# Kernel tuning notes

Hardware: AMD Instinct MI355X
Metric: run time of the kernel (lower is better)

## Reference

```python
import jax, jax.numpy as jnp
import numpy as np

HID = 128      # hidden_dim
HEADS = 8      # num_heads
PHD = 16       # per_head_dim
NTYPES = 3     # num_edge_types
N = 50000      # num nodes
E = 250000     # edges per edge type


def setup_inputs() -> dict:
    key = jax.random.key(0)
    ks = jax.random.split(key, 8)
    x = jax.random.normal(ks[0], (N, HID), dtype=jnp.float32)
    adj0 = jax.random.randint(ks[1], (E, 2), 0, N)
    adj1 = jax.random.randint(ks[2], (E, 2), 0, N)
    adj2 = jax.random.randint(ks[3], (E, 2), 0, N)
    # weights stored [in, out] so application is x @ W (same math as torch Linear)
    Wq = jax.random.normal(ks[4], (NTYPES, HID, HEADS * PHD), dtype=jnp.float32) * 0.05
    Wk = jax.random.normal(ks[5], (NTYPES, HID, HEADS * PHD), dtype=jnp.float32) * 0.05
    Wm = jax.random.normal(ks[6], (NTYPES, 2 * HID, HEADS * PHD), dtype=jnp.float32) * 0.05
    bm = jax.random.normal(ks[7], (NTYPES, HEADS * PHD), dtype=jnp.float32) * 0.01
    return {"x": x, "adj0": adj0, "adj1": adj1, "adj2": adj2,
            "Wq": Wq, "Wk": Wk, "Wm": Wm, "bm": bm}


def reference(x, adj0, adj1, adj2, Wq, Wk, Wm, bm):
    scale = PHD ** (-0.5)
    n = x.shape[0]
    msgs, scores, tgts = [], [], []
    for t, adj in enumerate((adj0, adj1, adj2)):
        src_r = x[adj[:, 0]]                       # [E, HID]
        tgt_r = x[adj[:, 1]]                       # [E, HID]
        pair = jnp.concatenate([src_r, tgt_r], axis=1)      # [E, 2*HID]
        m = jax.nn.relu(pair @ Wm[t] + bm[t]).reshape(-1, HEADS, PHD)
        q = (tgt_r @ Wq[t]).reshape(-1, HEADS, PHD) * scale
        k = (src_r @ Wk[t]).reshape(-1, HEADS, PHD)
        s = jnp.einsum('ehd,ehd->eh', q, k)        # [E, HEADS]
        msgs.append(m); scores.append(s); tgts.append(adj[:, 1])
    all_m = jnp.concatenate(msgs, axis=0)          # [TE, HEADS, PHD]
    all_s = jnp.concatenate(scores, axis=0)        # [TE, HEADS]
    all_t = jnp.concatenate(tgts, axis=0)          # [TE]
    # segment log-softmax over edges grouped by target node
    smax = jax.ops.segment_max(all_s, all_t, num_segments=n)        # [N, HEADS]
    shifted = all_s - smax[all_t]
    sumexp = jax.ops.segment_sum(jnp.exp(shifted), all_t, num_segments=n)
    logZ = jnp.log(jnp.where(sumexp > 0, sumexp, 1.0))
    probs = jnp.exp(shifted - logZ[all_t])                          # [TE, HEADS]
    agg = jax.ops.segment_sum(probs[..., None] * all_m, all_t, num_segments=n)
    return agg.reshape(n, HEADS * PHD)
```

## Files before the change

### kernel.cpp

```cpp
#include <hip/hip_runtime.h>

#define HID 128
#define NE 250000
#define NT 3
#define NN 50000
#define CAP 48
#define BPAD 136
#define PLANE (NN * 256)
#define GEMM_BLOCKS 391
#define EDGE_BLOCKS ((NT * NE + 511) / 512)

typedef unsigned int u32;
typedef unsigned short u16;
typedef __attribute__((ext_vector_type(8))) short short8;
typedef __attribute__((ext_vector_type(4))) float f32x4;

__device__ __forceinline__ u16 f2bf(float f) {
    u32 u = __float_as_uint(f);
    u += 0x7fffu + ((u >> 16) & 1u);
    return (u16)(u >> 16);
}
__device__ __forceinline__ float bflo(u32 u) { return __uint_as_float(u << 16); }
__device__ __forceinline__ float bfhi(u32 u) { return __uint_as_float(u & 0xffff0000u); }

__device__ __forceinline__ short8 pack8(const float4 a, const float4 b) {
    short8 r;
    r[0] = (short)f2bf(a.x); r[1] = (short)f2bf(a.y);
    r[2] = (short)f2bf(a.z); r[3] = (short)f2bf(a.w);
    r[4] = (short)f2bf(b.x); r[5] = (short)f2bf(b.y);
    r[6] = (short)f2bf(b.z); r[7] = (short)f2bf(b.w);
    return r;
}

__global__ __launch_bounds__(256)
void init_kernel(const float* __restrict__ Wq, const float* __restrict__ Wk,
                 const float* __restrict__ Wm,
                 u16* __restrict__ Wtb, u32* __restrict__ counts)
{
    const int b = blockIdx.x, tid = threadIdx.x;
    if (b < 768) {
        const int gid = b * 256 + tid;
        const int mat = gid >> 14;
        const int i   = gid & 16383;
        const int k   = i >> 7;
        const int n   = i & 127;
        const int t   = mat >> 2;
        const int m   = mat & 3;
        const float* src;
        if (m == 0)      src = Wq + (size_t)t * 16384;
        else if (m == 1) src = Wk + (size_t)t * 16384;
        else if (m == 2) src = Wm + (size_t)t * 32768;
        else             src = Wm + (size_t)t * 32768 + 16384;
        Wtb[(size_t)mat * 16384 + n * HID + k] = f2bf(src[i]);
    } else {
        const int gid = (b - 768) * 256 + tid;
        if (gid < NN / 4) {
            uint4 z; z.x = 0u; z.y = 0u; z.z = 0u; z.w = 0u;
            ((uint4*)counts)[gid] = z;
        }
    }
}

__global__ __launch_bounds__(512, 4)
void big_kernel(const float* __restrict__ x, const u16* __restrict__ Wtb,
                const float* __restrict__ bm,
                const int* __restrict__ a0, const int* __restrict__ a1,
                const int* __restrict__ a2,
                u32* __restrict__ counts, u32* __restrict__ edata,
                u16* __restrict__ P)
{
    __shared__ u16 Ws[128 * BPAD];
    const int b = blockIdx.x;
    const int tid = threadIdx.x;

    if (b >= GEMM_BLOCKS) {
        const int gid = (b - GEMM_BLOCKS) * 512 + tid;
        if (gid < NT * NE) {
            const int t = gid / NE, e = gid - t * NE;
            const int* adj = (t == 0) ? a0 : (t == 1) ? a1 : a2;
            const int2 pr = ((const int2*)adj)[e];
            const u32 pos = atomicAdd(&counts[pr.y], 1u);
            if (pos < CAP)
                edata[(size_t)pr.y * CAP + pos] = (u32)pr.x | ((u32)t << 16);
        }
        return;
    }

    const int wave = tid >> 6, lane = tid & 63;
    const int lm = lane & 15, quad = lane >> 4;
    const int r0 = b * 128 + wave * 16;
    const int ar = min(r0 + lm, NN - 1);
    const int node = r0 + lm;

    short8 Xf[4];
    #pragma unroll
    for (int ki = 0; ki < 4; ++ki) {
        const float* xp = x + (size_t)ar * HID + ki * 32 + quad * 8;
        Xf[ki] = pack8(*(const float4*)xp, *(const float4*)(xp + 4));
    }

    for (int mat = 0; mat < 12; ++mat) {
        const int t = mat >> 2, m = mat & 3;
        const u16* Wt = Wtb + (size_t)mat * 16384;

        __syncthreads();
        for (int c = tid; c < 2048; c += 512) {
            const int r = c >> 4, s = (c & 15) * 8;
            *(short8*)&Ws[r * BPAD + s] = *(const short8*)(Wt + r * HID + s);
        }
        __syncthreads();

        f32x4 acc[8];
        #pragma unroll
        for (int ct = 0; ct < 8; ++ct) acc[ct] = (f32x4){0.f, 0.f, 0.f, 0.f};
        #pragma unroll
        for (int ki = 0; ki < 4; ++ki) {
            #pragma unroll
            for (int ct = 0; ct < 8; ++ct) {
                const short8 Wf = *(const short8*)&Ws[(ct * 16 + lm) * BPAD + ki * 32 + quad * 8];
                acc[ct] = __builtin_amdgcn_mfma_f32_16x16x32_bf16(Wf, Xf[ki], acc[ct], 0, 0, 0);
            }
        }

        const int half = (m >= 2) ? 128 : 0;
        const int pidx = (m == 1 || m == 2) ? t : (3 + t);
        u16* Pd = P + (size_t)pidx * PLANE + half;
        if (node < NN) {
            #pragma unroll
            for (int ct = 0; ct < 8; ++ct) {
                const int oc = ct * 16 + quad * 4;
                float b0 = 0.f, b1 = 0.f, b2 = 0.f, b3 = 0.f;
                if (m == 3) {
                    const float4 bv = *(const float4*)(bm + t * HID + oc);
                    b0 = bv.x; b1 = bv.y; b2 = bv.z; b3 = bv.w;
                }
                uint2 pk;
                pk.x = (u32)f2bf(acc[ct][0] + b0) | ((u32)f2bf(acc[ct][1] + b1) << 16);
                pk.y = (u32)f2bf(acc[ct][2] + b2) | ((u32)f2bf(acc[ct][3] + b3) << 16);
                *(uint2*)(Pd + (size_t)node * 256 + oc) = pk;
            }
        }
    }
}

__global__ __launch_bounds__(256)
void gather_kernel(const u16* __restrict__ P, const u32* __restrict__ counts,
                   const u32* __restrict__ edata, float* __restrict__ out)
{
    const int wave = threadIdx.x >> 6, lane = threadIdx.x & 63;
    const int node = blockIdx.x * 4 + wave;
    if (node >= NN) return;
    const int j0 = lane * 2;

    const int dg = min((int)__builtin_amdgcn_readfirstlane((int)counts[node]), CAP);
    const int idxs = (lane < CAP) ? (int)edata[(size_t)node * CAP + lane] : 0;

    float q0[NT], q1[NT], b0[NT], b1[NT];
    #pragma unroll
    for (int t = 0; t < NT; ++t) {
        const u16* qb = P + (size_t)(3 + t) * PLANE + (size_t)node * 256;
        const u32 qv = *(const u32*)(qb + j0);
        const u32 bv = *(const u32*)(qb + 128 + j0);
        q0[t] = bflo(qv) * 0.25f;
        q1[t] = bfhi(qv) * 0.25f;
        b0[t] = bflo(bv);
        b1[t] = bfhi(bv);
    }

    float acc0 = 0.f, acc1 = 0.f, den = 0.f;
    for (int e = 0; e < dg; e += 12) {
        u32 kv[12], av[12];
        int ty[12];
        #pragma unroll
        for (int u = 0; u < 12; ++u) {
            int w = __builtin_amdgcn_readlane(idxs, e + u);
            w = (e + u < dg) ? w : 0;
            w = __builtin_amdgcn_readfirstlane(w);
            const int tt = w >> 16, s = w & 0xffff;
            ty[u] = tt;
            const u16* ka = P + (size_t)tt * PLANE + (size_t)s * 256;
            kv[u] = *(const u32*)(ka + j0);
            av[u] = *(const u32*)(ka + 128 + j0);
        }
        #pragma unroll
        for (int u = 0; u < 12; ++u) {
            const int tt = ty[u];
            const float cq0 = (tt == 0) ? q0[0] : (tt == 1) ? q0[1] : q0[2];
            const float cq1 = (tt == 0) ? q1[0] : (tt == 1) ? q1[1] : q1[2];
            const float cb0 = (tt == 0) ? b0[0] : (tt == 1) ? b0[1] : b0[2];
            const float cb1 = (tt == 0) ? b1[0] : (tt == 1) ? b1[1] : b1[2];
            float d = cq0 * bflo(kv[u]) + cq1 * bfhi(kv[u]);
            d += __shfl_xor(d, 1);
            d += __shfl_xor(d, 2);
            d += __shfl_xor(d, 4);
            float ex = __expf(d);
            ex = (e + u < dg) ? ex : 0.f;
            den  += ex;
            acc0 += ex * fmaxf(bflo(av[u]) + cb0, 0.f);
            acc1 += ex * fmaxf(bfhi(av[u]) + cb1, 0.f);
        }
    }

    const float inv = den > 0.f ? 1.f / den : 0.f;
    float2 o;
    o.x = acc0 * inv;
    o.y = acc1 * inv;
    *(float2*)(out + (size_t)node * HID + j0) = o;
}

extern "C" void kernel_launch(void* const* d_in, const int* in_sizes, int n_in,
                              void* d_out, int out_size, void* d_ws, size_t ws_size,
                              hipStream_t stream)
{
    const float* x  = (const float*)d_in[0];
    const int* a0   = (const int*)d_in[1];
    const int* a1   = (const int*)d_in[2];
    const int* a2   = (const int*)d_in[3];
    const float* Wq = (const float*)d_in[4];
    const float* Wk = (const float*)d_in[5];
    const float* Wm = (const float*)d_in[6];
    const float* bm = (const float*)d_in[7];
    float* out = (float*)d_out;

    const size_t planeB = (size_t)PLANE * sizeof(u16);
    char* p = (char*)d_ws;
    u16* P      = (u16*)p;  p += 6 * planeB;
    u16* Wtb    = (u16*)p;  p += 393216;
    u32* counts = (u32*)p;  p += 200000;
    u32* edata  = (u32*)p;

    init_kernel<<<768 + 49, 256, 0, stream>>>(Wq, Wk, Wm, Wtb, counts);
    big_kernel<<<GEMM_BLOCKS + EDGE_BLOCKS, 512, 0, stream>>>(
        x, Wtb, bm, a0, a1, a2, counts, edata, P);
    gather_kernel<<<(NN + 3) / 4, 256, 0, stream>>>(P, counts, edata, out);
}
```

Before: 228.3 us.

## Drop LDS weight staging; each wave computes 32 rows reading weights from global

The GEMM part of the fused kernel no longer copies each weight matrix into shared memory with block-wide barriers. Each wave now reads weight fragments straight from global/L2 and reuses each fragment for two 16-row node tiles, so the block shrinks to 256 threads covering the same 128 rows. This removes the per-matrix barriers and LDS traffic but puts more register pressure on each wave and makes weight loads depend on cache hits. The gather loop is also unrolled to batch 16 edges instead of 12, to keep more neighbor loads in flight.

Result: slower. 267.3 us (+17.1%).

```diff
diff --git a/kernel.cpp b/kernel.cpp
--- a/kernel.cpp
+++ b/kernel.cpp
@@ -5,10 +5,9 @@
 #define NT 3
 #define NN 50000
 #define CAP 48
-#define BPAD 136
 #define PLANE (NN * 256)
 #define GEMM_BLOCKS 391
-#define EDGE_BLOCKS ((NT * NE + 511) / 512)
+#define EDGE_BLOCKS ((NT * NE + 255) / 256)
 
 typedef unsigned int u32;
 typedef unsigned short u16;
@@ -61,7 +60,7 @@
     }
 }
 
-__global__ __launch_bounds__(512, 4)
+__global__ __launch_bounds__(256)
 void big_kernel(const float* __restrict__ x, const u16* __restrict__ Wtb,
                 const float* __restrict__ bm,
                 const int* __restrict__ a0, const int* __restrict__ a1,
@@ -69,12 +68,11 @@
                 u32* __restrict__ counts, u32* __restrict__ edata,
                 u16* __restrict__ P)
 {
-    __shared__ u16 Ws[128 * BPAD];
     const int b = blockIdx.x;
     const int tid = threadIdx.x;
 
     if (b >= GEMM_BLOCKS) {
-        const int gid = (b - GEMM_BLOCKS) * 512 + tid;
+        const int gid = (b - GEMM_BLOCKS) * 256 + tid;
         if (gid < NT * NE) {
             const int t = gid / NE, e = gid - t * NE;
             const int* adj = (t == 0) ? a0 : (t == 1) ? a1 : a2;
@@ -88,56 +86,59 @@
 
     const int wave = tid >> 6, lane = tid & 63;
     const int lm = lane & 15, quad = lane >> 4;
-    const int r0 = b * 128 + wave * 16;
-    const int ar = min(r0 + lm, NN - 1);
-    const int node = r0 + lm;
-
-    short8 Xf[4];
+    const int r0 = b * 128 + wave * 32;
+    const int ar0 = min(r0 + lm,      NN - 1);
+    const int ar1 = min(r0 + 16 + lm, NN - 1);
+
+    short8 Xf0[4], Xf1[4];
     #pragma unroll
     for (int ki = 0; ki < 4; ++ki) {
-        const float* xp = x + (size_t)ar * HID + ki * 32 + quad * 8;
-        Xf[ki] = pack8(*(const float4*)xp, *(const float4*)(xp + 4));
+        const float* xp0 = x + (size_t)ar0 * HID + ki * 32 + quad * 8;
+        const float* xp1 = x + (size_t)ar1 * HID + ki * 32 + quad * 8;
+        Xf0[ki] = pack8(*(const float4*)xp0, *(const float4*)(xp0 + 4));
+        Xf1[ki] = pack8(*(const float4*)xp1, *(const float4*)(xp1 + 4));
     }
 
     for (int mat = 0; mat < 12; ++mat) {
         const int t = mat >> 2, m = mat & 3;
-        const u16* Wt = Wtb + (size_t)mat * 16384;
-
-        __syncthreads();
-        for (int c = tid; c < 2048; c += 512) {
-            const int r = c >> 4, s = (c & 15) * 8;
-            *(short8*)&Ws[r * BPAD + s] = *(const short8*)(Wt + r * HID + s);
-        }
-        __syncthreads();
-
-        f32x4 acc[8];
-        #pragma unroll
-        for (int ct = 0; ct < 8; ++ct) acc[ct] = (f32x4){0.f, 0.f, 0.f, 0.f};
+        const u16* Wf0 = Wtb + (size_t)mat * 16384 + lm * HID + quad * 8;
+
+        f32x4 acc[8][2];
+        #pragma unroll
+        for (int ct = 0; ct < 8; ++ct) {
+            acc[ct][0] = (f32x4){0.f, 0.f, 0.f, 0.f};
+            acc[ct][1] = (f32x4){0.f, 0.f, 0.f, 0.f};
+        }
         #pragma unroll
         for (int ki = 0; ki < 4; ++ki) {
             #pragma unroll
             for (int ct = 0; ct < 8; ++ct) {
-                const short8 Wf = *(const short8*)&Ws[(ct * 16 + lm) * BPAD + ki * 32 + quad * 8];
-                acc[ct] = __builtin_amdgcn_mfma_f32_16x16x32_bf16(Wf, Xf[ki], acc[ct], 0, 0, 0);
+                const short8 Wf = *(const short8*)(Wf0 + ct * 16 * HID + ki * 32);
+                acc[ct][0] = __builtin_amdgcn_mfma_f32_16x16x32_bf16(Wf, Xf0[ki], acc[ct][0], 0, 0, 0);
+                acc[ct][1] = __builtin_amdgcn_mfma_f32_16x16x32_bf16(Wf, Xf1[ki], acc[ct][1], 0, 0, 0);
             }
         }
 
         const int half = (m >= 2) ? 128 : 0;
         const int pidx = (m == 1 || m == 2) ? t : (3 + t);
         u16* Pd = P + (size_t)pidx * PLANE + half;
-        if (node < NN) {
+        #pragma unroll
+        for (int ct = 0; ct < 8; ++ct) {
+            const int oc = ct * 16 + quad * 4;
+            float b0 = 0.f, b1 = 0.f, b2 = 0.f, b3 = 0.f;
+            if (m == 3) {
+                const float4 bv = *(const float4*)(bm + t * HID + oc);
+                b0 = bv.x; b1 = bv.y; b2 = bv.z; b3 = bv.w;
+            }
             #pragma unroll
-            for (int ct = 0; ct < 8; ++ct) {
-                const int oc = ct * 16 + quad * 4;
-                float b0 = 0.f, b1 = 0.f, b2 = 0.f, b3 = 0.f;
-                if (m == 3) {
-                    const float4 bv = *(const float4*)(bm + t * HID + oc);
-                    b0 = bv.x; b1 = bv.y; b2 = bv.z; b3 = bv.w;
+            for (int nt = 0; nt < 2; ++nt) {
+                const int node = r0 + nt * 16 + lm;
+                if (node < NN) {
+                    uint2 pk;
+                    pk.x = (u32)f2bf(acc[ct][nt][0] + b0) | ((u32)f2bf(acc[ct][nt][1] + b1) << 16);
+                    pk.y = (u32)f2bf(acc[ct][nt][2] + b2) | ((u32)f2bf(acc[ct][nt][3] + b3) << 16);
+                    *(uint2*)(Pd + (size_t)node * 256 + oc) = pk;
                 }
-                uint2 pk;
-                pk.x = (u32)f2bf(acc[ct][0] + b0) | ((u32)f2bf(acc[ct][1] + b1) << 16);
-                pk.y = (u32)f2bf(acc[ct][2] + b2) | ((u32)f2bf(acc[ct][3] + b3) << 16);
-                *(uint2*)(Pd + (size_t)node * 256 + oc) = pk;
             }
         }
     }
@@ -168,11 +169,11 @@
     }
 
     float acc0 = 0.f, acc1 = 0.f, den = 0.f;
-    for (int e = 0; e < dg; e += 12) {
-        u32 kv[12], av[12];
-        int ty[12];
-        #pragma unroll
-        for (int u = 0; u < 12; ++u) {
+    for (int e = 0; e < dg; e += 16) {
+        u32 kv[16], av[16];
+        int ty[16];
+        #pragma unroll
+        for (int u = 0; u < 16; ++u) {
             int w = __builtin_amdgcn_readlane(idxs, e + u);
             w = (e + u < dg) ? w : 0;
             w = __builtin_amdgcn_readfirstlane(w);
@@ -183,7 +184,7 @@
             av[u] = *(const u32*)(ka + 128 + j0);
         }
         #pragma unroll
-        for (int u = 0; u < 12; ++u) {
+        for (int u = 0; u < 16; ++u) {
             const int tt = ty[u];
             const float cq0 = (tt == 0) ? q0[0] : (tt == 1) ? q0[1] : q0[2];
             const float cq1 = (tt == 0) ? q1[0] : (tt == 1) ? q1[1] : q1[2];
@@ -230,7 +231,7 @@
     u32* edata  = (u32*)p;
 
     init_kernel<<<768 + 49, 256, 0, stream>>>(Wq, Wk, Wm, Wtb, counts);
-    big_kernel<<<GEMM_BLOCKS + EDGE_BLOCKS, 512, 0, stream>>>(
+    big_kernel<<<GEMM_BLOCKS + EDGE_BLOCKS, 256, 0, stream>>>(
         x, Wtb, bm, a0, a1, a2, counts, edata, P);
     gather_kernel<<<(NN + 3) / 4, 256, 0, stream>>>(P, counts, edata, out);
 }
```
